# Optimization experiments

Measured on AMD Instinct MI355X. Metric: run time of the kernel, lower is better.

Reference implementation:

```python
import jax, jax.numpy as jnp
import numpy as np

B, T, H, W, C = 8, 32, 64, 64, 3
F = 24        # conv filters
U = 128       # lstm units
O = 1         # output units

def _conv(x, w, b):
    # x: [N,H,W,Cin], w: [3,3,Cin,Cout], SAME padding, linear activation
    y = jax.lax.conv_general_dilated(x, w, window_strides=(1, 1), padding='SAME',
                                     dimension_numbers=('NHWC', 'HWIO', 'NHWC'))
    return y + b

def setup_inputs() -> dict:
    key = jax.random.key(0)
    ks = jax.random.split(key, 16)
    s = lambda *shape: 0.05
    inp = {
        'x': jax.random.normal(ks[0], (B, T, H, W, C), dtype=jnp.float32),
        'conv1_w': jax.random.normal(ks[1], (3, 3, C, F), dtype=jnp.float32) * 0.1,
        'conv1_b': jnp.zeros((F,), jnp.float32),
        'conv2_w': jax.random.normal(ks[2], (3, 3, F, F), dtype=jnp.float32) * 0.1,
        'conv2_b': jnp.zeros((F,), jnp.float32),
        'Wf': jax.random.normal(ks[3], (F + U, U), dtype=jnp.float32) * 0.08,
        'bf': jnp.zeros((U,), jnp.float32),
        'Wi': jax.random.normal(ks[4], (F + U, U), dtype=jnp.float32) * 0.08,
        'bi': jnp.zeros((U,), jnp.float32),
        'Wc': jax.random.normal(ks[5], (F + U, U), dtype=jnp.float32) * 0.08,
        'bc': jnp.zeros((U,), jnp.float32),
        'Wo': jax.random.normal(ks[6], (F + U, U), dtype=jnp.float32) * 0.08,
        'bo': jnp.zeros((U,), jnp.float32),
        'out_w': jax.random.normal(ks[7], (U, O), dtype=jnp.float32) * 0.08,
        'out_b': jnp.zeros((O,), jnp.float32),
    }
    return inp

def reference(x, conv1_w, conv1_b, conv2_w, conv2_b, Wf, bf, Wi, bi, Wc, bc, Wo, bo, out_w, out_b):
    b, t, h, w, c = x.shape
    # CNN block (per-frame): two linear 3x3 convs, no pooling inside block
    xr = x.reshape(b * t, h, w, c)
    xr = _conv(xr, conv1_w, conv1_b)
    xr = _conv(xr, conv2_w, conv2_b)
    # TimeDistributed(GlobalAvgPool2D): mean over H,W -> [B,T,F]
    feat = xr.reshape(b, t, h, w, -1).mean(axis=(2, 3))

    # custom LSTM recurrence over time via scan
    def step(carry, xt):
        hs, cs = carry
        z = jnp.concatenate([xt, hs], axis=-1)           # [B, F+U]
        f = jax.nn.sigmoid(z @ Wf + bf)
        i = jax.nn.sigmoid(z @ Wi + bi)
        g = jnp.tanh(z @ Wc + bc)
        o = jax.nn.sigmoid(z @ Wo + bo)
        c_new = cs * f + i * g
        h_new = jnp.tanh(c_new) * o
        return (h_new, c_new), h_new

    h0 = jnp.zeros((b, Wf.shape[1]), x.dtype)
    c0 = jnp.zeros((b, Wf.shape[1]), x.dtype)
    _, hs = jax.lax.scan(step, (h0, c0), jnp.swapaxes(feat, 0, 1))  # [T,B,U]
    hs = jnp.swapaxes(hs, 0, 1)                                     # [B,T,U]
    return hs @ out_w + out_b                                       # [B,T,O]
```

## Files before the change

kernel.cpp:

```cpp
#include <hip/hip_runtime.h>
#include <math.h>

#define Bb 8
#define Tt 32
#define Hh 64
#define Ww 64
#define Cc 3
#define Ff 24
#define Uu 128

typedef float v2f __attribute__((ext_vector_type(2)));

__device__ __forceinline__ float fast_sigmoid(float x) {
    float e = __builtin_amdgcn_exp2f(-1.442695040888963f * x);
    return __builtin_amdgcn_rcpf(1.f + e);
}
__device__ __forceinline__ float fast_tanh(float x) {
    float e = __builtin_amdgcn_exp2f(-2.885390081777927f * x);
    return 2.f * __builtin_amdgcn_rcpf(1.f + e) - 1.f;
}

__global__ void convfeat_kernel(const float* __restrict__ x,
                                const float* __restrict__ w1, const float* __restrict__ b1,
                                const float* __restrict__ w2, const float* __restrict__ b2,
                                float* __restrict__ feat) {
    int n = blockIdx.x;
    const float* xf = x + (size_t)n * (Hh * Ww * Cc);
    int tid  = threadIdx.x;
    int row  = tid >> 2;
    int part = tid & 3;

    __shared__ float partial[256][3];
    __shared__ float rowsum[64][3];
    __shared__ float colv[64][12];
    __shared__ float st[75];
    __shared__ float yst[24][9];

    float s0 = 0.f, s1 = 0.f, s2 = 0.f;
    const float4* p4 = (const float4*)(xf + (row * Ww + part * 16) * Cc);
#pragma unroll
    for (int i = 0; i < 12; ++i) {
        float4 v = p4[i];
        int j = i * 4;
        float vv[4] = {v.x, v.y, v.z, v.w};
#pragma unroll
        for (int l = 0; l < 4; ++l) {
            int c = (j + l) % 3;
            if (c == 0) s0 += vv[l]; else if (c == 1) s1 += vv[l]; else s2 += vv[l];
        }
    }
    partial[tid][0] = s0; partial[tid][1] = s1; partial[tid][2] = s2;

    if (tid < 64) {
        int r = tid;
#pragma unroll
        for (int w4 = 0; w4 < 4; ++w4) {
            int w = (w4 < 2) ? w4 : 60 + w4;
#pragma unroll
            for (int c = 0; c < 3; ++c) colv[r][w4 * 3 + c] = xf[(r * Ww + w) * Cc + c];
        }
    }
    __syncthreads();

    if (part == 0) {
#pragma unroll
        for (int c = 0; c < 3; ++c)
            rowsum[row][c] = partial[tid][c] + partial[tid + 1][c]
                           + partial[tid + 2][c] + partial[tid + 3][c];
    }
    __syncthreads();

    if (tid < 3) {
        float t = 0.f;
        for (int r = 0; r < 64; ++r) t += rowsum[r][tid];
        st[tid * 25 + 0] = t;
    }
    if (tid >= 4 && tid < 16) {
        int k = tid - 4; int ri = k / 3, c = k % 3;
        int r = (ri < 2) ? ri : 60 + ri;
        st[c * 25 + 1 + ri] = rowsum[r][c];
    }
    if (tid >= 64 && tid < 76) {
        int k = tid - 64;
        float t = 0.f;
        for (int r = 0; r < 64; ++r) t += colv[r][k];
        int wi = k / 3, c = k % 3;
        st[c * 25 + 5 + wi] = t;
    }
    if (tid >= 128 && tid < 176) {
        int k = tid - 128; int pos = k / 3, c = k % 3;
        int ri = pos >> 2, wi = pos & 3;
        int r = (ri < 2) ? ri : 60 + ri;
        int w = (wi < 2) ? wi : 60 + wi;
        st[c * 25 + 9 + pos] = xf[(r * Ww + w) * Cc + c];
    }
    __syncthreads();

    if (tid < 24) {
        int f = tid;
        float Sy = 0, r0 = 0, r63 = 0, c0 = 0, c63 = 0, y00 = 0, y0W = 0, yH0 = 0, yHW = 0;
        for (int c = 0; c < 3; ++c) {
            const float* S = st + c * 25;
            float Sx = S[0];
            float rX[4] = {S[1], S[2], S[3], S[4]};
            float cX[4] = {S[5], S[6], S[7], S[8]};
            const float* X = S + 9;
            #define W1(p, q) w1[(((p) * 3 + (q)) * 3 + c) * 24 + f]
#pragma unroll
            for (int p = 0; p < 3; ++p)
#pragma unroll
                for (int q = 0; q < 3; ++q) {
                    float t = Sx;
                    if (p == 0) t -= rX[3];
                    if (p == 2) t -= rX[0];
                    if (q == 0) t -= cX[3];
                    if (q == 2) t -= cX[0];
                    if (p == 0 && q == 0) t += X[3 * 4 + 3];
                    if (p == 0 && q == 2) t += X[3 * 4 + 0];
                    if (p == 2 && q == 0) t += X[0 * 4 + 3];
                    if (p == 2 && q == 2) t += X[0 * 4 + 0];
                    Sy += W1(p, q) * t;
                }
#pragma unroll
            for (int q = 0; q < 3; ++q) {
                float Rr0  = rX[0] - ((q == 0) ? X[0 * 4 + 3] : 0.f) - ((q == 2) ? X[0 * 4 + 0] : 0.f);
                float Rr1  = rX[1] - ((q == 0) ? X[1 * 4 + 3] : 0.f) - ((q == 2) ? X[1 * 4 + 0] : 0.f);
                float Rr62 = rX[2] - ((q == 0) ? X[2 * 4 + 3] : 0.f) - ((q == 2) ? X[2 * 4 + 0] : 0.f);
                float Rr63 = rX[3] - ((q == 0) ? X[3 * 4 + 3] : 0.f) - ((q == 2) ? X[3 * 4 + 0] : 0.f);
                r0  += W1(1, q) * Rr0  + W1(2, q) * Rr1;
                r63 += W1(0, q) * Rr62 + W1(1, q) * Rr63;
            }
#pragma unroll
            for (int p = 0; p < 3; ++p) {
                float Rc0  = cX[0] - ((p == 0) ? X[3 * 4 + 0] : 0.f) - ((p == 2) ? X[0 * 4 + 0] : 0.f);
                float Rc1  = cX[1] - ((p == 0) ? X[3 * 4 + 1] : 0.f) - ((p == 2) ? X[0 * 4 + 1] : 0.f);
                float Rc62 = cX[2] - ((p == 0) ? X[3 * 4 + 2] : 0.f) - ((p == 2) ? X[0 * 4 + 2] : 0.f);
                float Rc63 = cX[3] - ((p == 0) ? X[3 * 4 + 3] : 0.f) - ((p == 2) ? X[0 * 4 + 3] : 0.f);
                c0  += W1(p, 1) * Rc0  + W1(p, 2) * Rc1;
                c63 += W1(p, 0) * Rc62 + W1(p, 1) * Rc63;
            }
            y00 += W1(1, 1) * X[0 * 4 + 0] + W1(1, 2) * X[0 * 4 + 1]
                 + W1(2, 1) * X[1 * 4 + 0] + W1(2, 2) * X[1 * 4 + 1];
            y0W += W1(1, 0) * X[0 * 4 + 2] + W1(1, 1) * X[0 * 4 + 3]
                 + W1(2, 0) * X[1 * 4 + 2] + W1(2, 1) * X[1 * 4 + 3];
            yH0 += W1(0, 1) * X[2 * 4 + 0] + W1(0, 2) * X[2 * 4 + 1]
                 + W1(1, 1) * X[3 * 4 + 0] + W1(1, 2) * X[3 * 4 + 1];
            yHW += W1(0, 0) * X[2 * 4 + 2] + W1(0, 1) * X[2 * 4 + 3]
                 + W1(1, 0) * X[3 * 4 + 2] + W1(1, 1) * X[3 * 4 + 3];
            #undef W1
        }
        float bb = b1[f];
        yst[f][0] = Sy + 4096.f * bb;
        yst[f][1] = r0 + 64.f * bb;
        yst[f][2] = r63 + 64.f * bb;
        yst[f][3] = c0 + 64.f * bb;
        yst[f][4] = c63 + 64.f * bb;
        yst[f][5] = y00 + bb; yst[f][6] = y0W + bb;
        yst[f][7] = yH0 + bb; yst[f][8] = yHW + bb;
    }
    __syncthreads();

    if (tid < 24) {
        int g = tid;
        float acc = 0.f;
        for (int f = 0; f < 24; ++f) {
            float Sy = yst[f][0], rY0 = yst[f][1], rY63 = yst[f][2], cY0 = yst[f][3], cY63 = yst[f][4];
            float yc00 = yst[f][5], yc0W = yst[f][6], ycH0 = yst[f][7], ycHW = yst[f][8];
#pragma unroll
            for (int p = 0; p < 3; ++p)
#pragma unroll
                for (int q = 0; q < 3; ++q) {
                    float t = Sy;
                    if (p == 0) t -= rY63;
                    if (p == 2) t -= rY0;
                    if (q == 0) t -= cY63;
                    if (q == 2) t -= cY0;
                    if (p == 0 && q == 0) t += ycHW;
                    if (p == 0 && q == 2) t += ycH0;
                    if (p == 2 && q == 0) t += yc0W;
                    if (p == 2 && q == 2) t += yc00;
                    acc += w2[(((p * 3 + q) * 24 + f) * 24) + g] * t;
                }
        }
        feat[(size_t)n * 24 + g] = b2[g] + acc * (1.f / 4096.f);
    }
}

__global__ void gpre_kernel(const float* __restrict__ feat,
                            const float* __restrict__ Wf, const float* __restrict__ bf,
                            const float* __restrict__ Wi, const float* __restrict__ bi,
                            const float* __restrict__ Wc, const float* __restrict__ bc,
                            const float* __restrict__ Wo, const float* __restrict__ bo,
                            float* __restrict__ G) {
    int blk = blockIdx.x;
    int t = blk >> 3, b = blk & 7;
    int tid = threadIdx.x;
    int g = tid >> 7, u = tid & 127;
    const float* W    = (g == 0) ? Wf : (g == 1) ? Wi : (g == 2) ? Wc : Wo;
    const float* bias = (g == 0) ? bf : (g == 1) ? bi : (g == 2) ? bc : bo;
    int n = b * Tt + t;
    float acc = bias[u];
#pragma unroll
    for (int k = 0; k < Ff; ++k) acc += feat[(size_t)n * Ff + k] * W[k * Uu + u];
    G[(size_t)blk * 512 + tid] = acc;
}

__global__ __launch_bounds__(1024, 4) void lstm_kernel(
        const float* __restrict__ G,
        const float* __restrict__ Wf, const float* __restrict__ Wi,
        const float* __restrict__ Wc, const float* __restrict__ Wo,
        const float* __restrict__ out_w, const float* __restrict__ out_b,
        float* __restrict__ out) {
    int b   = blockIdx.x;
    int tid = threadIdx.x;
    int up  = tid & 63;
    int g   = (tid >> 6) & 3;
    int q   = tid >> 8;
    const float* Wg = (g == 0) ? Wf : (g == 1) ? Wi : (g == 2) ? Wc : Wo;

    const float* wbase = Wg + (size_t)(Ff + 32 * q) * Uu + 2 * up;
#define LDW(i) v2f w##i = *(const v2f*)(wbase + (size_t)(i) * Uu)
    LDW(0);  LDW(1);  LDW(2);  LDW(3);  LDW(4);  LDW(5);  LDW(6);  LDW(7);
    LDW(8);  LDW(9);  LDW(10); LDW(11); LDW(12); LDW(13); LDW(14); LDW(15);
    LDW(16); LDW(17); LDW(18); LDW(19); LDW(20); LDW(21); LDW(22); LDW(23);
    LDW(24); LDW(25); LDW(26); LDW(27); LDW(28); LDW(29); LDW(30); LDW(31);
#undef LDW

    __shared__ float hs[Uu];
    __shared__ float part[16][Uu];
    __shared__ float hist[Tt][Uu];

    float cs = 0.f;
    if (tid < Uu) hs[tid] = 0.f;
    __syncthreads();

    for (int t = 0; t < Tt; ++t) {
        float g0 = 0.f, g1 = 0.f, g2 = 0.f, g3 = 0.f;
        if (tid < Uu) {
            const float* Gt = G + ((size_t)(t * Bb + b)) * 512 + tid;
            g0 = Gt[0]; g1 = Gt[128]; g2 = Gt[256]; g3 = Gt[384];
        }

        v2f ae = {0.f, 0.f}, ao = {0.f, 0.f};
        const v2f* hp = (const v2f*)(hs + q * 32);
#define FMA2(j, we, wo_) { v2f h2 = hp[j]; \
        asm("v_pk_fma_f32 %0, %1, %2, %0 op_sel:[0,0,0] op_sel_hi:[1,0,1]" \
            : "+v"(ae) : "v"(we), "v"(h2)); \
        asm("v_pk_fma_f32 %0, %1, %2, %0 op_sel:[0,1,0] op_sel_hi:[1,1,1]" \
            : "+v"(ao) : "v"(wo_), "v"(h2)); }
        FMA2(0,  w0,  w1);  FMA2(1,  w2,  w3);
        FMA2(2,  w4,  w5);  FMA2(3,  w6,  w7);
        FMA2(4,  w8,  w9);  FMA2(5,  w10, w11);
        FMA2(6,  w12, w13); FMA2(7,  w14, w15);
        FMA2(8,  w16, w17); FMA2(9,  w18, w19);
        FMA2(10, w20, w21); FMA2(11, w22, w23);
        FMA2(12, w24, w25); FMA2(13, w26, w27);
        FMA2(14, w28, w29); FMA2(15, w30, w31);
#undef FMA2
        v2f acc = ae + ao;
        *(v2f*)&part[q * 4 + g][2 * up] = acc;
        __syncthreads();

        if (tid < Uu) {
            int u = tid;
            float sf = part[0][u] + part[4][u] + part[8][u]  + part[12][u] + g0;
            float si = part[1][u] + part[5][u] + part[9][u]  + part[13][u] + g1;
            float sg = part[2][u] + part[6][u] + part[10][u] + part[14][u] + g2;
            float so = part[3][u] + part[7][u] + part[11][u] + part[15][u] + g3;
            float f  = fast_sigmoid(sf);
            float i  = fast_sigmoid(si);
            float gg = fast_tanh(sg);
            float o  = fast_sigmoid(so);
            cs = cs * f + i * gg;
            float hn = fast_tanh(cs) * o;
            hs[u] = hn;
            hist[t][u] = hn;
        }
        __syncthreads();
    }

    int tt = tid >> 5, j = tid & 31;
    const float4* hh = (const float4*)(&hist[tt][j * 4]);
    float4 a0 = hh[0];
    const float* owp = out_w + j * 4;
    float pw = a0.x * owp[0] + a0.y * owp[1] + a0.z * owp[2] + a0.w * owp[3];
#pragma unroll
    for (int off = 16; off > 0; off >>= 1) pw += __shfl_down(pw, off, 32);
    if (j == 0) out[b * Tt + tt] = pw + out_b[0];
}

extern "C" void kernel_launch(void* const* d_in, const int* in_sizes, int n_in,
                              void* d_out, int out_size, void* d_ws, size_t ws_size,
                              hipStream_t stream) {
    const float* x   = (const float*)d_in[0];
    const float* w1  = (const float*)d_in[1];
    const float* b1  = (const float*)d_in[2];
    const float* w2  = (const float*)d_in[3];
    const float* b2  = (const float*)d_in[4];
    const float* Wf  = (const float*)d_in[5];
    const float* bf  = (const float*)d_in[6];
    const float* Wi  = (const float*)d_in[7];
    const float* bi  = (const float*)d_in[8];
    const float* Wc  = (const float*)d_in[9];
    const float* bc  = (const float*)d_in[10];
    const float* Wo  = (const float*)d_in[11];
    const float* bo  = (const float*)d_in[12];
    const float* ow  = (const float*)d_in[13];
    const float* ob  = (const float*)d_in[14];
    float* out = (float*)d_out;

    float* ws   = (float*)d_ws;
    float* feat = ws;
    float* G    = ws + 6144;

    convfeat_kernel<<<Bb * Tt, 256, 0, stream>>>(x, w1, b1, w2, b2, feat);
    gpre_kernel<<<Bb * Tt, 512, 0, stream>>>(feat, Wf, bf, Wi, bi, Wc, bc, Wo, bo, G);
    lstm_kernel<<<Bb, 1024, 0, stream>>>(G, Wf, Wi, Wc, Wo, ow, ob, out);
}
```

Measured before the change: 45.40 us.

## Fuse gate pre-projection into conv kernel and prefetch next-step gates in LSTM

Folds the gpre kernel into the conv-feature kernel: each block keeps its 24 features in shared memory and computes the 512 input-gate pre-activations directly, removing a launch and a global round trip of the features. The LSTM loop now prefetches the next timestep's G values one iteration ahead so the global load latency overlaps with the recurrent FMA work. It also relaxes launch bounds and pins the weight registers with empty asm so they stay in VGPRs. The conv kernel does more work per block, and the register pinning may raise register pressure.

New measurement: 45.61 us. No clear change (+0.5%).

```diff
diff --git a/kernel.cpp b/kernel.cpp
--- a/kernel.cpp
+++ b/kernel.cpp
@@ -23,7 +23,11 @@
 __global__ void convfeat_kernel(const float* __restrict__ x,
                                 const float* __restrict__ w1, const float* __restrict__ b1,
                                 const float* __restrict__ w2, const float* __restrict__ b2,
-                                float* __restrict__ feat) {
+                                const float* __restrict__ Wf, const float* __restrict__ bf,
+                                const float* __restrict__ Wi, const float* __restrict__ bi,
+                                const float* __restrict__ Wc, const float* __restrict__ bc,
+                                const float* __restrict__ Wo, const float* __restrict__ bo,
+                                float* __restrict__ G) {
     int n = blockIdx.x;
     const float* xf = x + (size_t)n * (Hh * Ww * Cc);
     int tid  = threadIdx.x;
@@ -35,6 +39,7 @@
     __shared__ float colv[64][12];
     __shared__ float st[75];
     __shared__ float yst[24][9];
+    __shared__ float feats[24];
 
     float s0 = 0.f, s1 = 0.f, s2 = 0.f;
     const float4* p4 = (const float4*)(xf + (row * Ww + part * 16) * Cc);
@@ -182,30 +187,26 @@
                     acc += w2[(((p * 3 + q) * 24 + f) * 24) + g] * t;
                 }
         }
-        feat[(size_t)n * 24 + g] = b2[g] + acc * (1.f / 4096.f);
-    }
-}
-
-__global__ void gpre_kernel(const float* __restrict__ feat,
-                            const float* __restrict__ Wf, const float* __restrict__ bf,
-                            const float* __restrict__ Wi, const float* __restrict__ bi,
-                            const float* __restrict__ Wc, const float* __restrict__ bc,
-                            const float* __restrict__ Wo, const float* __restrict__ bo,
-                            float* __restrict__ G) {
-    int blk = blockIdx.x;
-    int t = blk >> 3, b = blk & 7;
-    int tid = threadIdx.x;
-    int g = tid >> 7, u = tid & 127;
-    const float* W    = (g == 0) ? Wf : (g == 1) ? Wi : (g == 2) ? Wc : Wo;
-    const float* bias = (g == 0) ? bf : (g == 1) ? bi : (g == 2) ? bc : bo;
-    int n = b * Tt + t;
-    float acc = bias[u];
-#pragma unroll
-    for (int k = 0; k < Ff; ++k) acc += feat[(size_t)n * Ff + k] * W[k * Uu + u];
-    G[(size_t)blk * 512 + tid] = acc;
-}
-
-__global__ __launch_bounds__(1024, 4) void lstm_kernel(
+        feats[g] = b2[g] + acc * (1.f / 4096.f);
+    }
+    __syncthreads();
+
+    int b = n >> 5, t = n & 31;
+    float* Gdst = G + ((size_t)(t * Bb + b)) * 512;
+#pragma unroll
+    for (int rep = 0; rep < 2; ++rep) {
+        int col = tid + rep * 256;
+        int gg = col >> 7, u = col & 127;
+        const float* W    = (gg == 0) ? Wf : (gg == 1) ? Wi : (gg == 2) ? Wc : Wo;
+        const float* bias = (gg == 0) ? bf : (gg == 1) ? bi : (gg == 2) ? bc : bo;
+        float acc = bias[u];
+#pragma unroll
+        for (int k = 0; k < Ff; ++k) acc += feats[k] * W[k * Uu + u];
+        Gdst[col] = acc;
+    }
+}
+
+__global__ __launch_bounds__(1024) void lstm_kernel(
         const float* __restrict__ G,
         const float* __restrict__ Wf, const float* __restrict__ Wi,
         const float* __restrict__ Wc, const float* __restrict__ Wo,
@@ -225,6 +226,13 @@
     LDW(16); LDW(17); LDW(18); LDW(19); LDW(20); LDW(21); LDW(22); LDW(23);
     LDW(24); LDW(25); LDW(26); LDW(27); LDW(28); LDW(29); LDW(30); LDW(31);
 #undef LDW
+#define KA8(a,b_,c,d,e,f,g_,h) asm volatile("" : "+v"(a),"+v"(b_),"+v"(c),\
+        "+v"(d),"+v"(e),"+v"(f),"+v"(g_),"+v"(h))
+    KA8(w0,  w1,  w2,  w3,  w4,  w5,  w6,  w7);
+    KA8(w8,  w9,  w10, w11, w12, w13, w14, w15);
+    KA8(w16, w17, w18, w19, w20, w21, w22, w23);
+    KA8(w24, w25, w26, w27, w28, w29, w30, w31);
+#undef KA8
 
     __shared__ float hs[Uu];
     __shared__ float part[16][Uu];
@@ -232,13 +240,19 @@
 
     float cs = 0.f;
     if (tid < Uu) hs[tid] = 0.f;
+
+    float gc0 = 0.f, gc1 = 0.f, gc2 = 0.f, gc3 = 0.f;
+    if (tid < Uu) {
+        const float* Gt = G + ((size_t)(0 * Bb + b)) * 512 + tid;
+        gc0 = Gt[0]; gc1 = Gt[128]; gc2 = Gt[256]; gc3 = Gt[384];
+    }
     __syncthreads();
 
     for (int t = 0; t < Tt; ++t) {
-        float g0 = 0.f, g1 = 0.f, g2 = 0.f, g3 = 0.f;
-        if (tid < Uu) {
-            const float* Gt = G + ((size_t)(t * Bb + b)) * 512 + tid;
-            g0 = Gt[0]; g1 = Gt[128]; g2 = Gt[256]; g3 = Gt[384];
+        float gn0 = 0.f, gn1 = 0.f, gn2 = 0.f, gn3 = 0.f;
+        if (tid < Uu && t + 1 < Tt) {
+            const float* Gt = G + ((size_t)((t + 1) * Bb + b)) * 512 + tid;
+            gn0 = Gt[0]; gn1 = Gt[128]; gn2 = Gt[256]; gn3 = Gt[384];
         }
 
         v2f ae = {0.f, 0.f}, ao = {0.f, 0.f};
@@ -263,10 +277,10 @@
 
         if (tid < Uu) {
             int u = tid;
-            float sf = part[0][u] + part[4][u] + part[8][u]  + part[12][u] + g0;
-            float si = part[1][u] + part[5][u] + part[9][u]  + part[13][u] + g1;
-            float sg = part[2][u] + part[6][u] + part[10][u] + part[14][u] + g2;
-            float so = part[3][u] + part[7][u] + part[11][u] + part[15][u] + g3;
+            float sf = part[0][u] + part[4][u] + part[8][u]  + part[12][u] + gc0;
+            float si = part[1][u] + part[5][u] + part[9][u]  + part[13][u] + gc1;
+            float sg = part[2][u] + part[6][u] + part[10][u] + part[14][u] + gc2;
+            float so = part[3][u] + part[7][u] + part[11][u] + part[15][u] + gc3;
             float f  = fast_sigmoid(sf);
             float i  = fast_sigmoid(si);
             float gg = fast_tanh(sg);
@@ -276,6 +290,7 @@
             hs[u] = hn;
             hist[t][u] = hn;
         }
+        gc0 = gn0; gc1 = gn1; gc2 = gn2; gc3 = gn3;
         __syncthreads();
     }
 
@@ -309,11 +324,9 @@
     const float* ob  = (const float*)d_in[14];
     float* out = (float*)d_out;
 
-    float* ws   = (float*)d_ws;
-    float* feat = ws;
-    float* G    = ws + 6144;
-
-    convfeat_kernel<<<Bb * Tt, 256, 0, stream>>>(x, w1, b1, w2, b2, feat);
-    gpre_kernel<<<Bb * Tt, 512, 0, stream>>>(feat, Wf, bf, Wi, bi, Wc, bc, Wo, bo, G);
+    float* G = (float*)d_ws;
+
+    convfeat_kernel<<<Bb * Tt, 256, 0, stream>>>(x, w1, b1, w2, b2,
+                                                 Wf, bf, Wi, bi, Wc, bc, Wo, bo, G);
     lstm_kernel<<<Bb, 1024, 0, stream>>>(G, Wf, Wi, Wc, Wo, ow, ob, out);
 }
```
